# Kernel tuning notes

Measured on AMD Instinct MI355X. Metric: run time of the kernel, lower is better.

Reference implementation:

```python
import jax, jax.numpy as jnp
import numpy as np

N = 100000   # nodes
E = 3200000  # edges per graph
D = 16       # embedding_size, num_heads = 1
ATTN_SLOPE = 0.2   # DGL GATv2Conv negative_slope default
ACT_SLOPE = 0.01   # torch.nn.functional.leaky_relu default (activation arg)


def gatv2_layer(h, src, dst, W_src, b_src, W_dst, b_dst, attn):
    """DGL GATv2Conv with num_heads=1, activation=leaky_relu.
    h: [N, D]; src/dst: [E] int; W_*: [D, D]; b_*: [D]; attn: [D].
    """
    feat_src = h @ W_src + b_src          # [N, D]
    feat_dst = h @ W_dst + b_dst          # [N, D]
    el = feat_src[src]                    # [E, D] gather to edges
    e = jax.nn.leaky_relu(el + feat_dst[dst], ATTN_SLOPE)  # [E, D]
    score = e @ attn                      # [E] attention logits
    # segment softmax over incoming edges of each destination node
    smax = jax.ops.segment_max(score, dst, num_segments=N)
    smax = jnp.where(jnp.isfinite(smax), smax, 0.0)  # empty segments -> 0
    ex = jnp.exp(score - smax[dst])       # [E]
    denom = jax.ops.segment_sum(ex, dst, num_segments=N)  # [N]
    alpha = ex / denom[dst]               # [E]
    rst = jax.ops.segment_sum(alpha[:, None] * el, dst, num_segments=N)  # [N, D]
    return jax.nn.leaky_relu(rst, ACT_SLOPE)


def setup_inputs() -> dict:
    key = jax.random.key(0)
    ks = jax.random.split(key, 16)
    s = 1.0 / np.sqrt(D)
    return {
        "embedding": jax.random.normal(ks[0], (N, D), jnp.float32),
        "src1": jax.random.randint(ks[1], (E,), 0, N, jnp.int32),
        "dst1": jax.random.randint(ks[2], (E,), 0, N, jnp.int32),
        "src2": jax.random.randint(ks[3], (E,), 0, N, jnp.int32),
        "dst2": jax.random.randint(ks[4], (E,), 0, N, jnp.int32),
        "W_src1": jax.random.normal(ks[5], (D, D), jnp.float32) * s,
        "b_src1": jnp.zeros((D,), jnp.float32),
        "W_dst1": jax.random.normal(ks[6], (D, D), jnp.float32) * s,
        "b_dst1": jnp.zeros((D,), jnp.float32),
        "attn1": jax.random.normal(ks[7], (D,), jnp.float32) * s,
        "W_src2": jax.random.normal(ks[8], (D, D), jnp.float32) * s,
        "b_src2": jnp.zeros((D,), jnp.float32),
        "W_dst2": jax.random.normal(ks[9], (D, D), jnp.float32) * s,
        "b_dst2": jnp.zeros((D,), jnp.float32),
        "attn2": jax.random.normal(ks[10], (D,), jnp.float32) * s,
    }


def reference(embedding, src1, dst1, src2, dst2,
              W_src1, b_src1, W_dst1, b_dst1, attn1,
              W_src2, b_src2, W_dst2, b_dst2, attn2):
    user2item = gatv2_layer(embedding, src1, dst1, W_src1, b_src1, W_dst1, b_dst1, attn1)
    item_influence = gatv2_layer(user2item, src2, dst2, W_src2, b_src2, W_dst2, b_dst2, attn2)
    return item_influence  # [N, D]
```

## Files before the change

kernel.cpp:

```cpp
#include <hip/hip_runtime.h>
#include <hip/hip_fp16.h>

#define D 16
#define R 64
#define RBITS 6
#define RMASK 63
#define STRIDE 2560
#define CAP 2560
#define ACCT 512
#define KPT (CAP / ACCT)
#define EPB 16384
#define CHK 8192
#define K1T 1024
#define NB2 1664
#define ATTN_SLOPE 0.2f
#define ACT_SLOPE 0.01f

__device__ __forceinline__ float leaky_a(float v) {
    return v > 0.f ? v : ATTN_SLOPE * v;
}
__device__ __forceinline__ float2 h2f(unsigned u) {
    __half2 h = *(__half2*)&u;
    return __half22float2(h);
}


__device__ void binscatter_tile(int tile, const int* __restrict__ src,
                                const int* __restrict__ dst,
                                int* __restrict__ gcur, unsigned* __restrict__ binned,
                                int E, int NB, char* sb) {
    unsigned* sorted = (unsigned*)sb;
    unsigned short* sposb = (unsigned short*)(sb + 32768);
    int* soffs = (int*)(sb + 49152);
    int* wcur = (int*)(sb + 49152 + 4 * NB2);
    int* swsum = (int*)(sb + 49152 + 8 * NB2);
    int tid = threadIdx.x;
    int lane = tid & 63, w = tid >> 6;
    int base = tile * EPB;
    int count = E - base;
    if (count > EPB) count = EPB;

    for (int i = tid; i < NB; i += K1T) wcur[i] = 0;
    __syncthreads();

    if (count == EPB) {
        const int4* d4 = (const int4*)(dst + base);
#pragma unroll
        for (int m = 0; m < 4; m++) {
            int4 a = d4[m * K1T + tid];
            atomicAdd(&wcur[a.x >> RBITS], 1);
            atomicAdd(&wcur[a.y >> RBITS], 1);
            atomicAdd(&wcur[a.z >> RBITS], 1);
            atomicAdd(&wcur[a.w >> RBITS], 1);
        }
    } else {
        for (int k = 0; k < 16; k++) {
            int e = base + k * K1T + tid;
            if (e < E) atomicAdd(&wcur[dst[e] >> RBITS], 1);
        }
    }
    __syncthreads();

    for (int i = tid; i < NB; i += K1T) {
        int c = wcur[i];
        if (c > 0) {
            int res = atomicAdd(&gcur[i], c);
            wcur[i] = i * STRIDE + res;
        }
    }
    __syncthreads();

    int i0 = 2 * tid, i1 = 2 * tid + 1;
    for (int c = 0; c < 2; c++) {
        int cbase = base + c * CHK;
        int cc = count - c * CHK;
        if (cc <= 0) break;
        if (cc > CHK) cc = CHK;
        bool full = (cc == CHK);

        for (int i = tid; i < NB; i += K1T) soffs[i] = 0;
        __syncthreads();

        if (full) {
            const int4* d4 = (const int4*)(dst + cbase);
            int4 a = d4[tid], b4 = d4[K1T + tid];
            atomicAdd(&soffs[a.x >> RBITS], 1);
            atomicAdd(&soffs[a.y >> RBITS], 1);
            atomicAdd(&soffs[a.z >> RBITS], 1);
            atomicAdd(&soffs[a.w >> RBITS], 1);
            atomicAdd(&soffs[b4.x >> RBITS], 1);
            atomicAdd(&soffs[b4.y >> RBITS], 1);
            atomicAdd(&soffs[b4.z >> RBITS], 1);
            atomicAdd(&soffs[b4.w >> RBITS], 1);
        } else {
            for (int k = 0; k < 8; k++) {
                int e = cbase + k * K1T + tid;
                if (e < E) atomicAdd(&soffs[dst[e] >> RBITS], 1);
            }
        }
        __syncthreads();

        int a0 = (i0 < NB) ? soffs[i0] : 0;
        int a1 = (i1 < NB) ? soffs[i1] : 0;
        int pair = a0 + a1;
        int x = pair;
#pragma unroll
        for (int ofs = 1; ofs < 64; ofs <<= 1) {
            int y = __shfl_up(x, ofs, 64);
            if (lane >= ofs) x += y;
        }
        if (lane == 63) swsum[w] = x;
        __syncthreads();
        if (w == 0) {
            int v = (lane < 16) ? swsum[lane] : 0;
            int s = v;
#pragma unroll
            for (int ofs = 1; ofs < 16; ofs <<= 1) {
                int y = __shfl_up(s, ofs, 64);
                if (lane >= ofs) s += y;
            }
            if (lane < 16) swsum[lane] = s - v;
        }
        __syncthreads();
        int excl = x - pair + swsum[w];
        int e0 = excl, e1 = excl + a0;
        int d0v = 0, d1v = 0;
        if (i0 < NB) {
            soffs[i0] = e0;
            if (a0 > 0) { d0v = wcur[i0] - e0; wcur[i0] = d0v; }
        }
        if (i1 < NB) {
            soffs[i1] = e1;
            if (a1 > 0) { d1v = wcur[i1] - e1; wcur[i1] = d1v; }
        }
        __syncthreads();

        if (full) {
            const int4* d4 = (const int4*)(dst + cbase);
            const int4* s4 = (const int4*)(src + cbase);
            int4 a = d4[tid], b4 = d4[K1T + tid];
            int4 sa = s4[tid], sb4 = s4[K1T + tid];
            int dd[8] = {a.x, a.y, a.z, a.w, b4.x, b4.y, b4.z, b4.w};
            int ss[8] = {sa.x, sa.y, sa.z, sa.w, sb4.x, sb4.y, sb4.z, sb4.w};
#pragma unroll
            for (int m = 0; m < 8; m++) {
                int bb = dd[m] >> RBITS;
                int r = atomicAdd(&soffs[bb], 1);
                sorted[r] = ((unsigned)ss[m] << RBITS) | (unsigned)(dd[m] & RMASK);
                sposb[r] = (unsigned short)bb;
            }
        } else {
            for (int k = 0; k < 8; k++) {
                int e = cbase + k * K1T + tid;
                if (e < E) {
                    int dv = dst[e];
                    int bb = dv >> RBITS;
                    int r = atomicAdd(&soffs[bb], 1);
                    sorted[r] = ((unsigned)src[e] << RBITS) | (unsigned)(dv & RMASK);
                    sposb[r] = (unsigned short)bb;
                }
            }
        }
        __syncthreads();

#pragma unroll
        for (int m = 0; m < 8; m++) {
            int p = m * K1T + tid;
            if (p < cc) {
                int bb = sposb[p];
                int pos = p + wcur[bb];
                if (pos < (bb + 1) * STRIDE) binned[pos] = sorted[p];
            }
        }
        __syncthreads();

        if (c == 0) {
            if (i0 < NB && a0 > 0) wcur[i0] = d0v + e0 + a0;
            if (i1 < NB && a1 > 0) wcur[i1] = d1v + e1 + a1;
            __syncthreads();
        }
    }
}

__device__ void transform_tile(int tile, const float* __restrict__ h,
                               const float* __restrict__ Ws, const float* __restrict__ bs,
                               const float* __restrict__ Wd, const float* __restrict__ bd,
                               __half* __restrict__ fsh, float* __restrict__ fdst,
                               int N, char* sb) {
    float* sWs = (float*)sb;
    float* sWd = sWs + 256;
    float* sbs = sWd + 256;
    float* sbd = sbs + 16;
    int t = threadIdx.x;
    if (t < 256) { sWs[t] = Ws[t]; sWd[t] = Wd[t]; }
    if (t < 16) { sbs[t] = bs[t]; sbd[t] = bd[t]; }
    __syncthreads();
    int n = tile * K1T + t;
    if (n >= N) return;
    float hv[D];
    const float4* h4 = (const float4*)(h + (size_t)n * D);
#pragma unroll
    for (int k = 0; k < 4; k++) {
        float4 v = h4[k];
        hv[4 * k] = v.x; hv[4 * k + 1] = v.y; hv[4 * k + 2] = v.z; hv[4 * k + 3] = v.w;
    }
    float os[D], od[D];
#pragma unroll
    for (int d = 0; d < D; d++) {
        float ss = sbs[d];
        float sd = sbd[d];
#pragma unroll
        for (int k = 0; k < D; k++) {
            ss += hv[k] * sWs[k * D + d];
            sd += hv[k] * sWd[k * D + d];
        }
        os[d] = ss; od[d] = sd;
    }
    unsigned us[8];
#pragma unroll
    for (int k = 0; k < 8; k++) {
        __half2 hh = __floats2half2_rn(os[2 * k], os[2 * k + 1]);
        us[k] = *(unsigned*)&hh;
    }
    uint4* fo = (uint4*)(fsh + (size_t)n * D);
    fo[0] = make_uint4(us[0], us[1], us[2], us[3]);
    fo[1] = make_uint4(us[4], us[5], us[6], us[7]);
    float4* fd4 = (float4*)(fdst + (size_t)n * D);
#pragma unroll
    for (int k = 0; k < 4; k++)
        fd4[k] = make_float4(od[4 * k], od[4 * k + 1], od[4 * k + 2], od[4 * k + 3]);
}

__global__ void __launch_bounds__(K1T)
k1_kernel(const float* h, const float* Ws, const float* bs,
          const float* Wd, const float* bd,
          __half* fsh, float* fdst,
          const int* srcA, const int* dstA, int* gA, unsigned* binnedA, int EA,
          const int* srcB, const int* dstB, int* gB, unsigned* binnedB, int EB,
          int N, int NB, int B1, int B2, int TT) {
    __shared__ __align__(16) char sb[49152 + 8 * NB2 + 64];
    int bid = blockIdx.x;
    if (bid < B1) {
        binscatter_tile(bid, srcA, dstA, gA, binnedA, EA, NB, sb);
    } else if (bid < B1 + B2) {
        binscatter_tile(bid - B1, srcB, dstB, gB, binnedB, EB, NB, sb);
    } else {
        int t = bid - B1 - B2;
        if (t < TT) transform_tile(t, h, Ws, bs, Wd, bd, fsh, fdst, N, sb);
    }
}


template <bool DO_TAIL>
__global__ void __launch_bounds__(ACCT)
acc_kernel(const unsigned* __restrict__ binned, const int* __restrict__ gcur,
           const __half* __restrict__ fsh, const float* __restrict__ fdst,
           const float* __restrict__ attn, float* __restrict__ out,
           __half* __restrict__ fs2h, float* __restrict__ fd2,
           const float* __restrict__ Ws2, const float* __restrict__ bs2,
           const float* __restrict__ Wd2, const float* __restrict__ bd2,
           int N) {
    __shared__ float sfd[R * D];
    __shared__ int ebuf[CAP];
    __shared__ float exbuf[CAP];
    __shared__ int cstart[R + 1];
    __shared__ int cur[R];
    __shared__ float wtail[544];
    int b = blockIdx.x;
    int tid = threadIdx.x;
    int node0 = b * R;
    int nn = N - node0;
    if (nn > R) nn = R;
    for (int i = tid; i < nn * D; i += ACCT) sfd[i] = fdst[node0 * D + i];
    if (tid <= R) cstart[tid] = 0;
    if (DO_TAIL) {
        if (tid < 256) { wtail[tid] = Ws2[tid]; wtail[256 + tid] = Wd2[tid]; }
        if (tid < 16) { wtail[512 + tid] = bs2[tid]; wtail[528 + tid] = bd2[tid]; }
    }

    float av[D];
#pragma unroll
    for (int k = 0; k < D; k++) av[k] = attn[k];

    int cnt = gcur[b];
    if (cnt > CAP) cnt = CAP;
    int base = b * STRIDE;

    unsigned pls[KPT];
#pragma unroll
    for (int k = 0; k < KPT; k++) {
        int j = k * ACCT + tid;
        pls[k] = (j < cnt) ? binned[base + j] : 0xFFFFFFFFu;
    }
    __syncthreads();

    const uint4* fsh4 = (const uint4*)fsh;
    const uint2* fsq = (const uint2*)fsh;
    const float4* sfd4 = (const float4*)sfd;

#pragma unroll
    for (int k = 0; k < KPT; k++)
        if (pls[k] != 0xFFFFFFFFu) atomicAdd(&cstart[pls[k] & RMASK], 1);

    float exs[KPT];
#pragma unroll
    for (int k = 0; k + 1 < KPT; k += 2) {
        unsigned q0 = pls[k], q1 = pls[k + 1];
        uint4 ua0, ub0, ua1, ub1;
        if (q0 != 0xFFFFFFFFu) {
            int s = q0 >> RBITS;
            ua0 = fsh4[2 * s]; ub0 = fsh4[2 * s + 1];
        }
        if (q1 != 0xFFFFFFFFu) {
            int s = q1 >> RBITS;
            ua1 = fsh4[2 * s]; ub1 = fsh4[2 * s + 1];
        }
        if (q0 != 0xFFFFFFFFu) {
            int loc = q0 & RMASK;
            float4 f0 = sfd4[loc * 4 + 0], f1 = sfd4[loc * 4 + 1];
            float4 f2 = sfd4[loc * 4 + 2], f3 = sfd4[loc * 4 + 3];
            float2 c0 = h2f(ua0.x), c1 = h2f(ua0.y), c2 = h2f(ua0.z), c3 = h2f(ua0.w);
            float2 c4 = h2f(ub0.x), c5 = h2f(ub0.y), c6 = h2f(ub0.z), c7 = h2f(ub0.w);
            float p = leaky_a(c0.x + f0.x) * av[0]  + leaky_a(c0.y + f0.y) * av[1]
                    + leaky_a(c1.x + f0.z) * av[2]  + leaky_a(c1.y + f0.w) * av[3]
                    + leaky_a(c2.x + f1.x) * av[4]  + leaky_a(c2.y + f1.y) * av[5]
                    + leaky_a(c3.x + f1.z) * av[6]  + leaky_a(c3.y + f1.w) * av[7]
                    + leaky_a(c4.x + f2.x) * av[8]  + leaky_a(c4.y + f2.y) * av[9]
                    + leaky_a(c5.x + f2.z) * av[10] + leaky_a(c5.y + f2.w) * av[11]
                    + leaky_a(c6.x + f3.x) * av[12] + leaky_a(c6.y + f3.y) * av[13]
                    + leaky_a(c7.x + f3.z) * av[14] + leaky_a(c7.y + f3.w) * av[15];
            exs[k] = __expf(p);
        }
        if (q1 != 0xFFFFFFFFu) {
            int loc = q1 & RMASK;
            float4 f0 = sfd4[loc * 4 + 0], f1 = sfd4[loc * 4 + 1];
            float4 f2 = sfd4[loc * 4 + 2], f3 = sfd4[loc * 4 + 3];
            float2 c0 = h2f(ua1.x), c1 = h2f(ua1.y), c2 = h2f(ua1.z), c3 = h2f(ua1.w);
            float2 c4 = h2f(ub1.x), c5 = h2f(ub1.y), c6 = h2f(ub1.z), c7 = h2f(ub1.w);
            float p = leaky_a(c0.x + f0.x) * av[0]  + leaky_a(c0.y + f0.y) * av[1]
                    + leaky_a(c1.x + f0.z) * av[2]  + leaky_a(c1.y + f0.w) * av[3]
                    + leaky_a(c2.x + f1.x) * av[4]  + leaky_a(c2.y + f1.y) * av[5]
                    + leaky_a(c3.x + f1.z) * av[6]  + leaky_a(c3.y + f1.w) * av[7]
                    + leaky_a(c4.x + f2.x) * av[8]  + leaky_a(c4.y + f2.y) * av[9]
                    + leaky_a(c5.x + f2.z) * av[10] + leaky_a(c5.y + f2.w) * av[11]
                    + leaky_a(c6.x + f3.x) * av[12] + leaky_a(c6.y + f3.y) * av[13]
                    + leaky_a(c7.x + f3.z) * av[14] + leaky_a(c7.y + f3.w) * av[15];
            exs[k + 1] = __expf(p);
        }
    }
    if (KPT & 1) {
        unsigned q0 = pls[KPT - 1];
        if (q0 != 0xFFFFFFFFu) {
            int s = q0 >> RBITS;
            uint4 ua0 = fsh4[2 * s], ub0 = fsh4[2 * s + 1];
            int loc = q0 & RMASK;
            float4 f0 = sfd4[loc * 4 + 0], f1 = sfd4[loc * 4 + 1];
            float4 f2 = sfd4[loc * 4 + 2], f3 = sfd4[loc * 4 + 3];
            float2 c0 = h2f(ua0.x), c1 = h2f(ua0.y), c2 = h2f(ua0.z), c3 = h2f(ua0.w);
            float2 c4 = h2f(ub0.x), c5 = h2f(ub0.y), c6 = h2f(ub0.z), c7 = h2f(ub0.w);
            float p = leaky_a(c0.x + f0.x) * av[0]  + leaky_a(c0.y + f0.y) * av[1]
                    + leaky_a(c1.x + f0.z) * av[2]  + leaky_a(c1.y + f0.w) * av[3]
                    + leaky_a(c2.x + f1.x) * av[4]  + leaky_a(c2.y + f1.y) * av[5]
                    + leaky_a(c3.x + f1.z) * av[6]  + leaky_a(c3.y + f1.w) * av[7]
                    + leaky_a(c4.x + f2.x) * av[8]  + leaky_a(c4.y + f2.y) * av[9]
                    + leaky_a(c5.x + f2.z) * av[10] + leaky_a(c5.y + f2.w) * av[11]
                    + leaky_a(c6.x + f3.x) * av[12] + leaky_a(c6.y + f3.y) * av[13]
                    + leaky_a(c7.x + f3.z) * av[14] + leaky_a(c7.y + f3.w) * av[15];
            exs[KPT - 1] = __expf(p);
        }
    }
    __syncthreads();
    if (tid < R) {
        int v = cstart[tid];
        int x = v;
#pragma unroll
        for (int ofs = 1; ofs < 64; ofs <<= 1) {
            int y = __shfl_up(x, ofs, 64);
            if (tid >= ofs) x += y;
        }
        cstart[tid] = x - v;
        cur[tid] = x - v;
        if (tid == R - 1) cstart[R] = x;
    }
    __syncthreads();
#pragma unroll
    for (int k = 0; k < KPT; k++) {
        unsigned pl = pls[k];
        if (pl != 0xFFFFFFFFu) {
            int r = atomicAdd(&cur[pl & RMASK], 1);
            ebuf[r] = (int)pl;
            exbuf[r] = exs[k];
        }
    }
    __syncthreads();

    int lane = tid & 63;
    int w = tid >> 6;
    int q = lane & 3;
    int s2 = (lane >> 2) & 3;
    int n2 = lane >> 4;

    float4 acc[2];
    float den[2];
#pragma unroll
    for (int i = 0; i < 2; i++) {
        acc[i] = make_float4(0.f, 0.f, 0.f, 0.f);
        den[i] = 0.f;
    }
#pragma unroll
    for (int i = 0; i < 2; i++) {
        int loc = w * 8 + i * 4 + n2;
        int kb = cstart[loc], ke = cstart[loc + 1];
        int k = kb + s2;
        for (; k + 12 < ke; k += 16) {
            int pl0 = ebuf[k];
            int pl1 = ebuf[k + 4];
            int pl2 = ebuf[k + 8];
            int pl3 = ebuf[k + 12];
            float ex0 = exbuf[k];
            float ex1 = exbuf[k + 4];
            float ex2 = exbuf[k + 8];
            float ex3 = exbuf[k + 12];
            uint2 u0 = fsq[(((unsigned)pl0) >> RBITS) * 4 + q];
            uint2 u1 = fsq[(((unsigned)pl1) >> RBITS) * 4 + q];
            uint2 u2 = fsq[(((unsigned)pl2) >> RBITS) * 4 + q];
            uint2 u3 = fsq[(((unsigned)pl3) >> RBITS) * 4 + q];
            float2 a01 = h2f(u0.x), a23 = h2f(u0.y);
            float2 b01 = h2f(u1.x), b23 = h2f(u1.y);
            float2 c01 = h2f(u2.x), c23 = h2f(u2.y);
            float2 d01 = h2f(u3.x), d23 = h2f(u3.y);
            acc[i].x += ex0 * a01.x + ex1 * b01.x + ex2 * c01.x + ex3 * d01.x;
            acc[i].y += ex0 * a01.y + ex1 * b01.y + ex2 * c01.y + ex3 * d01.y;
            acc[i].z += ex0 * a23.x + ex1 * b23.x + ex2 * c23.x + ex3 * d23.x;
            acc[i].w += ex0 * a23.y + ex1 * b23.y + ex2 * c23.y + ex3 * d23.y;
            den[i] += (ex0 + ex1) + (ex2 + ex3);
        }
        for (; k < ke; k += 4) {
            int pl = ebuf[k];
            float ex = exbuf[k];
            uint2 u = fsq[(((unsigned)pl) >> RBITS) * 4 + q];
            float2 a01 = h2f(u.x), a23 = h2f(u.y);
            acc[i].x += ex * a01.x;
            acc[i].y += ex * a01.y;
            acc[i].z += ex * a23.x;
            acc[i].w += ex * a23.y;
            den[i] += ex;
        }
    }
#pragma unroll
    for (int i = 0; i < 2; i++) {
        float4 a = acc[i];
        float dn = den[i];
#pragma unroll
        for (int m = 4; m <= 8; m <<= 1) {
            a.x += __shfl_xor(a.x, m, 16);
            a.y += __shfl_xor(a.y, m, 16);
            a.z += __shfl_xor(a.z, m, 16);
            a.w += __shfl_xor(a.w, m, 16);
            dn += __shfl_xor(dn, m, 16);
        }
        int loc = w * 8 + i * 4 + n2;
        if (s2 == 0 && loc < nn) {
            float inv = dn > 0.f ? 1.f / dn : 0.f;
            float4 v;
            v.x = a.x * inv; v.x = v.x > 0.f ? v.x : ACT_SLOPE * v.x;
            v.y = a.y * inv; v.y = v.y > 0.f ? v.y : ACT_SLOPE * v.y;
            v.z = a.z * inv; v.z = v.z > 0.f ? v.z : ACT_SLOPE * v.z;
            v.w = a.w * inv; v.w = v.w > 0.f ? v.w : ACT_SLOPE * v.w;
            if (DO_TAIL) {
                *(float4*)&sfd[loc * D + q * 4] = v;
            } else {
                ((float4*)out)[(size_t)(node0 + loc) * 4 + q] = v;
            }
        }
    }
    if (DO_TAIL) {
        __syncthreads();
        int loc = tid >> 2, qq = tid & 3;
        if (tid < 256 && loc < nn) {
            float hvv[16];
#pragma unroll
            for (int k = 0; k < 16; k++) hvv[k] = sfd[loc * D + k];
            float s0 = wtail[512 + 4 * qq], s1 = wtail[513 + 4 * qq];
            float s2v = wtail[514 + 4 * qq], s3 = wtail[515 + 4 * qq];
            float d0 = wtail[528 + 4 * qq], d1 = wtail[529 + 4 * qq];
            float d2v = wtail[530 + 4 * qq], d3 = wtail[531 + 4 * qq];
#pragma unroll
            for (int k = 0; k < 16; k++) {
                float hk = hvv[k];
                const float* wr = &wtail[k * 16 + 4 * qq];
                const float* wr2 = &wtail[256 + k * 16 + 4 * qq];
                s0 += hk * wr[0]; s1 += hk * wr[1]; s2v += hk * wr[2]; s3 += hk * wr[3];
                d0 += hk * wr2[0]; d1 += hk * wr2[1]; d2v += hk * wr2[2]; d3 += hk * wr2[3];
            }
            __half2 p0 = __floats2half2_rn(s0, s1), p1 = __floats2half2_rn(s2v, s3);
            *(uint2*)(fs2h + (size_t)(node0 + loc) * D + 4 * qq) =
                make_uint2(*(unsigned*)&p0, *(unsigned*)&p1);
            *(float4*)(fd2 + (size_t)(node0 + loc) * D + 4 * qq) =
                make_float4(d0, d1, d2v, d3);
        }
    }
}


extern "C" void kernel_launch(void* const* d_in, const int* in_sizes, int n_in,
                              void* d_out, int out_size, void* d_ws, size_t ws_size,
                              hipStream_t stream) {
    const float* emb = (const float*)d_in[0];
    const int* src1 = (const int*)d_in[1];
    const int* dst1 = (const int*)d_in[2];
    const int* src2 = (const int*)d_in[3];
    const int* dst2 = (const int*)d_in[4];
    const float* Wsrc1 = (const float*)d_in[5];
    const float* bsrc1 = (const float*)d_in[6];
    const float* Wdst1 = (const float*)d_in[7];
    const float* bdst1 = (const float*)d_in[8];
    const float* attn1 = (const float*)d_in[9];
    const float* Wsrc2 = (const float*)d_in[10];
    const float* bsrc2 = (const float*)d_in[11];
    const float* Wdst2 = (const float*)d_in[12];
    const float* bdst2 = (const float*)d_in[13];
    const float* attn2 = (const float*)d_in[14];

    const int N = in_sizes[0] / D;
    const int E1 = in_sizes[1];
    const int E2 = in_sizes[3];
    const int NB = (N + R - 1) / R;
    const size_t ndf = (size_t)N * D;

    float* ws = (float*)d_ws;
    float* fd1 = ws;
    float* fd2 = fd1 + ndf;
    __half* fs1h = (__half*)(fd2 + ndf);
    __half* fs2h = fs1h + ndf;
    int* gA = (int*)(fs2h + ndf);
    int* gB = gA + NB2;
    unsigned* binned1 = (unsigned*)(gB + NB2);
    unsigned* binned2big = binned1 + (size_t)NB * STRIDE;
    size_t bigNeed = (size_t)((char*)(binned2big + (size_t)NB * STRIDE) - (char*)d_ws);
    bool big = ws_size >= bigNeed;
    (void)n_in; (void)out_size;

    const int B1 = (E1 + EPB - 1) / EPB;
    const int B2 = (E2 + EPB - 1) / EPB;
    const int TT = (N + K1T - 1) / K1T;

    (void)hipMemsetAsync(gA, 0, 2 * NB2 * sizeof(int), stream);

    if (big) {
        k1_kernel<<<B1 + B2 + TT, K1T, 0, stream>>>(
            emb, Wsrc1, bsrc1, Wdst1, bdst1, fs1h, fd1,
            src1, dst1, gA, binned1, E1,
            src2, dst2, gB, binned2big, E2,
            N, NB, B1, B2, TT);
        acc_kernel<true><<<NB, ACCT, 0, stream>>>(
            binned1, gA, fs1h, fd1, attn1, nullptr,
            fs2h, fd2, Wsrc2, bsrc2, Wdst2, bdst2, N);
        acc_kernel<false><<<NB, ACCT, 0, stream>>>(
            binned2big, gB, fs2h, fd2, attn2, (float*)d_out,
            nullptr, nullptr, nullptr, nullptr, nullptr, nullptr, N);
    } else {
        k1_kernel<<<B1 + TT, K1T, 0, stream>>>(
            emb, Wsrc1, bsrc1, Wdst1, bdst1, fs1h, fd1,
            src1, dst1, gA, binned1, E1,
            src2, dst2, gB, binned1, 0,
            N, NB, B1, 0, TT);
        acc_kernel<true><<<NB, ACCT, 0, stream>>>(
            binned1, gA, fs1h, fd1, attn1, nullptr,
            fs2h, fd2, Wsrc2, bsrc2, Wdst2, bdst2, N);
        k1_kernel<<<B2, K1T, 0, stream>>>(
            emb, Wsrc1, bsrc1, Wdst1, bdst1, fs1h, fd1,
            src2, dst2, gB, binned1, E2,
            src2, dst2, gB, binned1, 0,
            N, NB, B2, 0, 0);
        acc_kernel<false><<<NB, ACCT, 0, stream>>>(
            binned1, gB, fs2h, fd2, attn2, (float*)d_out,
            nullptr, nullptr, nullptr, nullptr, nullptr, nullptr, N);
    }
}
```

Baseline: 235.2 us.

## Halve binscatter block size and cache dst/src indices in registers

The binning kernel drops from 1024 to 512 threads per block, with a launch-bounds minimum of 4 blocks. Each thread now loads its 32 dst indices and 16 src indices per chunk once into registers and reuses them across the histogram and scatter passes, instead of re-reading them from global memory. The block-wide scan now gives each thread four bins, and each transform block handles 2048 nodes with a per-thread loop. Holding these arrays in registers raises register pressure, and with the launch-bounds limit this could cause spills.

```diff
diff --git a/kernel.cpp b/kernel.cpp
--- a/kernel.cpp
+++ b/kernel.cpp
@@ -11,7 +11,8 @@
 #define KPT (CAP / ACCT)
 #define EPB 16384
 #define CHK 8192
-#define K1T 1024
+#define K1T 512
+#define TNODES 2048
 #define NB2 1664
 #define ATTN_SLOPE 0.2f
 #define ACT_SLOPE 0.01f
@@ -39,22 +40,26 @@
     int base = tile * EPB;
     int count = E - base;
     if (count > EPB) count = EPB;
-
+    bool fullT = (count == EPB);
+
+    int dreg[32];
+    if (fullT) {
+        const int4* d4 = (const int4*)(dst + base);
+#pragma unroll
+        for (int m = 0; m < 8; m++) {
+            int4 a = d4[m * K1T + tid];
+            dreg[4 * m + 0] = a.x; dreg[4 * m + 1] = a.y;
+            dreg[4 * m + 2] = a.z; dreg[4 * m + 3] = a.w;
+        }
+    }
     for (int i = tid; i < NB; i += K1T) wcur[i] = 0;
     __syncthreads();
 
-    if (count == EPB) {
-        const int4* d4 = (const int4*)(dst + base);
-#pragma unroll
-        for (int m = 0; m < 4; m++) {
-            int4 a = d4[m * K1T + tid];
-            atomicAdd(&wcur[a.x >> RBITS], 1);
-            atomicAdd(&wcur[a.y >> RBITS], 1);
-            atomicAdd(&wcur[a.z >> RBITS], 1);
-            atomicAdd(&wcur[a.w >> RBITS], 1);
-        }
+    if (fullT) {
+#pragma unroll
+        for (int m = 0; m < 32; m++) atomicAdd(&wcur[dreg[m] >> RBITS], 1);
     } else {
-        for (int k = 0; k < 16; k++) {
+        for (int k = 0; k < 32; k++) {
             int e = base + k * K1T + tid;
             if (e < E) atomicAdd(&wcur[dst[e] >> RBITS], 1);
         }
@@ -70,30 +75,33 @@
     }
     __syncthreads();
 
-    int i0 = 2 * tid, i1 = 2 * tid + 1;
+    int i0 = 4 * tid;
     for (int c = 0; c < 2; c++) {
         int cbase = base + c * CHK;
         int cc = count - c * CHK;
         if (cc <= 0) break;
         if (cc > CHK) cc = CHK;
-        bool full = (cc == CHK);
-
+        bool fullC = fullT;
+
+        int sreg[16];
+        if (fullC) {
+            const int4* s4 = (const int4*)(src + cbase);
+#pragma unroll
+            for (int m2 = 0; m2 < 4; m2++) {
+                int4 a = s4[m2 * K1T + tid];
+                sreg[4 * m2 + 0] = a.x; sreg[4 * m2 + 1] = a.y;
+                sreg[4 * m2 + 2] = a.z; sreg[4 * m2 + 3] = a.w;
+            }
+        }
         for (int i = tid; i < NB; i += K1T) soffs[i] = 0;
         __syncthreads();
 
-        if (full) {
-            const int4* d4 = (const int4*)(dst + cbase);
-            int4 a = d4[tid], b4 = d4[K1T + tid];
-            atomicAdd(&soffs[a.x >> RBITS], 1);
-            atomicAdd(&soffs[a.y >> RBITS], 1);
-            atomicAdd(&soffs[a.z >> RBITS], 1);
-            atomicAdd(&soffs[a.w >> RBITS], 1);
-            atomicAdd(&soffs[b4.x >> RBITS], 1);
-            atomicAdd(&soffs[b4.y >> RBITS], 1);
-            atomicAdd(&soffs[b4.z >> RBITS], 1);
-            atomicAdd(&soffs[b4.w >> RBITS], 1);
+        if (fullC) {
+#pragma unroll
+            for (int mm = 0; mm < 16; mm++)
+                atomicAdd(&soffs[dreg[16 * c + mm] >> RBITS], 1);
         } else {
-            for (int k = 0; k < 8; k++) {
+            for (int k = 0; k < 16; k++) {
                 int e = cbase + k * K1T + tid;
                 if (e < E) atomicAdd(&soffs[dst[e] >> RBITS], 1);
             }
@@ -101,9 +109,11 @@
         __syncthreads();
 
         int a0 = (i0 < NB) ? soffs[i0] : 0;
-        int a1 = (i1 < NB) ? soffs[i1] : 0;
-        int pair = a0 + a1;
-        int x = pair;
+        int a1 = (i0 + 1 < NB) ? soffs[i0 + 1] : 0;
+        int a2 = (i0 + 2 < NB) ? soffs[i0 + 2] : 0;
+        int a3 = (i0 + 3 < NB) ? soffs[i0 + 3] : 0;
+        int quad = a0 + a1 + a2 + a3;
+        int x = quad;
 #pragma unroll
         for (int ofs = 1; ofs < 64; ofs <<= 1) {
             int y = __shfl_up(x, ofs, 64);
@@ -112,45 +122,48 @@
         if (lane == 63) swsum[w] = x;
         __syncthreads();
         if (w == 0) {
-            int v = (lane < 16) ? swsum[lane] : 0;
+            int v = (lane < 8) ? swsum[lane] : 0;
             int s = v;
 #pragma unroll
-            for (int ofs = 1; ofs < 16; ofs <<= 1) {
+            for (int ofs = 1; ofs < 8; ofs <<= 1) {
                 int y = __shfl_up(s, ofs, 64);
                 if (lane >= ofs) s += y;
             }
-            if (lane < 16) swsum[lane] = s - v;
-        }
-        __syncthreads();
-        int excl = x - pair + swsum[w];
-        int e0 = excl, e1 = excl + a0;
-        int d0v = 0, d1v = 0;
+            if (lane < 8) swsum[lane] = s - v;
+        }
+        __syncthreads();
+        int excl = x - quad + swsum[w];
+        int e0 = excl, e1 = e0 + a0, e2 = e1 + a1, e3 = e2 + a2;
+        int d0v = 0, d1v = 0, d2v = 0, d3v = 0;
         if (i0 < NB) {
             soffs[i0] = e0;
             if (a0 > 0) { d0v = wcur[i0] - e0; wcur[i0] = d0v; }
         }
-        if (i1 < NB) {
-            soffs[i1] = e1;
-            if (a1 > 0) { d1v = wcur[i1] - e1; wcur[i1] = d1v; }
-        }
-        __syncthreads();
-
-        if (full) {
-            const int4* d4 = (const int4*)(dst + cbase);
-            const int4* s4 = (const int4*)(src + cbase);
-            int4 a = d4[tid], b4 = d4[K1T + tid];
-            int4 sa = s4[tid], sb4 = s4[K1T + tid];
-            int dd[8] = {a.x, a.y, a.z, a.w, b4.x, b4.y, b4.z, b4.w};
-            int ss[8] = {sa.x, sa.y, sa.z, sa.w, sb4.x, sb4.y, sb4.z, sb4.w};
-#pragma unroll
-            for (int m = 0; m < 8; m++) {
-                int bb = dd[m] >> RBITS;
+        if (i0 + 1 < NB) {
+            soffs[i0 + 1] = e1;
+            if (a1 > 0) { d1v = wcur[i0 + 1] - e1; wcur[i0 + 1] = d1v; }
+        }
+        if (i0 + 2 < NB) {
+            soffs[i0 + 2] = e2;
+            if (a2 > 0) { d2v = wcur[i0 + 2] - e2; wcur[i0 + 2] = d2v; }
+        }
+        if (i0 + 3 < NB) {
+            soffs[i0 + 3] = e3;
+            if (a3 > 0) { d3v = wcur[i0 + 3] - e3; wcur[i0 + 3] = d3v; }
+        }
+        __syncthreads();
+
+        if (fullC) {
+#pragma unroll
+            for (int mm = 0; mm < 16; mm++) {
+                int dv = dreg[16 * c + mm];
+                int bb = dv >> RBITS;
                 int r = atomicAdd(&soffs[bb], 1);
-                sorted[r] = ((unsigned)ss[m] << RBITS) | (unsigned)(dd[m] & RMASK);
+                sorted[r] = ((unsigned)sreg[mm] << RBITS) | (unsigned)(dv & RMASK);
                 sposb[r] = (unsigned short)bb;
             }
         } else {
-            for (int k = 0; k < 8; k++) {
+            for (int k = 0; k < 16; k++) {
                 int e = cbase + k * K1T + tid;
                 if (e < E) {
                     int dv = dst[e];
@@ -164,8 +177,8 @@
         __syncthreads();
 
 #pragma unroll
-        for (int m = 0; m < 8; m++) {
-            int p = m * K1T + tid;
+        for (int mm = 0; mm < 16; mm++) {
+            int p = mm * K1T + tid;
             if (p < cc) {
                 int bb = sposb[p];
                 int pos = p + wcur[bb];
@@ -176,7 +189,9 @@
 
         if (c == 0) {
             if (i0 < NB && a0 > 0) wcur[i0] = d0v + e0 + a0;
-            if (i1 < NB && a1 > 0) wcur[i1] = d1v + e1 + a1;
+            if (i0 + 1 < NB && a1 > 0) wcur[i0 + 1] = d1v + e1 + a1;
+            if (i0 + 2 < NB && a2 > 0) wcur[i0 + 2] = d2v + e2 + a2;
+            if (i0 + 3 < NB && a3 > 0) wcur[i0 + 3] = d3v + e3 + a3;
             __syncthreads();
         }
     }
@@ -195,43 +210,46 @@
     if (t < 256) { sWs[t] = Ws[t]; sWd[t] = Wd[t]; }
     if (t < 16) { sbs[t] = bs[t]; sbd[t] = bd[t]; }
     __syncthreads();
-    int n = tile * K1T + t;
-    if (n >= N) return;
-    float hv[D];
-    const float4* h4 = (const float4*)(h + (size_t)n * D);
-#pragma unroll
-    for (int k = 0; k < 4; k++) {
-        float4 v = h4[k];
-        hv[4 * k] = v.x; hv[4 * k + 1] = v.y; hv[4 * k + 2] = v.z; hv[4 * k + 3] = v.w;
-    }
-    float os[D], od[D];
-#pragma unroll
-    for (int d = 0; d < D; d++) {
-        float ss = sbs[d];
-        float sd = sbd[d];
-#pragma unroll
-        for (int k = 0; k < D; k++) {
-            ss += hv[k] * sWs[k * D + d];
-            sd += hv[k] * sWd[k * D + d];
-        }
-        os[d] = ss; od[d] = sd;
-    }
-    unsigned us[8];
-#pragma unroll
-    for (int k = 0; k < 8; k++) {
-        __half2 hh = __floats2half2_rn(os[2 * k], os[2 * k + 1]);
-        us[k] = *(unsigned*)&hh;
-    }
-    uint4* fo = (uint4*)(fsh + (size_t)n * D);
-    fo[0] = make_uint4(us[0], us[1], us[2], us[3]);
-    fo[1] = make_uint4(us[4], us[5], us[6], us[7]);
-    float4* fd4 = (float4*)(fdst + (size_t)n * D);
-#pragma unroll
-    for (int k = 0; k < 4; k++)
-        fd4[k] = make_float4(od[4 * k], od[4 * k + 1], od[4 * k + 2], od[4 * k + 3]);
-}
-
-__global__ void __launch_bounds__(K1T)
+#pragma unroll
+    for (int kk = 0; kk < 4; kk++) {
+        int n = tile * TNODES + kk * K1T + t;
+        if (n >= N) break;
+        float hv[D];
+        const float4* h4 = (const float4*)(h + (size_t)n * D);
+#pragma unroll
+        for (int k = 0; k < 4; k++) {
+            float4 v = h4[k];
+            hv[4 * k] = v.x; hv[4 * k + 1] = v.y; hv[4 * k + 2] = v.z; hv[4 * k + 3] = v.w;
+        }
+        float os[D], od[D];
+#pragma unroll
+        for (int d = 0; d < D; d++) {
+            float ss = sbs[d];
+            float sd = sbd[d];
+#pragma unroll
+            for (int k = 0; k < D; k++) {
+                ss += hv[k] * sWs[k * D + d];
+                sd += hv[k] * sWd[k * D + d];
+            }
+            os[d] = ss; od[d] = sd;
+        }
+        unsigned us[8];
+#pragma unroll
+        for (int k = 0; k < 8; k++) {
+            __half2 hh = __floats2half2_rn(os[2 * k], os[2 * k + 1]);
+            us[k] = *(unsigned*)&hh;
+        }
+        uint4* fo = (uint4*)(fsh + (size_t)n * D);
+        fo[0] = make_uint4(us[0], us[1], us[2], us[3]);
+        fo[1] = make_uint4(us[4], us[5], us[6], us[7]);
+        float4* fd4 = (float4*)(fdst + (size_t)n * D);
+#pragma unroll
+        for (int k = 0; k < 4; k++)
+            fd4[k] = make_float4(od[4 * k], od[4 * k + 1], od[4 * k + 2], od[4 * k + 3]);
+    }
+}
+
+__global__ void __launch_bounds__(K1T, 4)
 k1_kernel(const float* h, const float* Ws, const float* bs,
           const float* Wd, const float* bd,
           __half* fsh, float* fdst,
@@ -543,7 +561,7 @@
 
     const int B1 = (E1 + EPB - 1) / EPB;
     const int B2 = (E2 + EPB - 1) / EPB;
-    const int TT = (N + K1T - 1) / K1T;
+    const int TT = (N + TNODES - 1) / TNODES;
 
     (void)hipMemsetAsync(gA, 0, 2 * NB2 * sizeof(int), stream);
 
```

Result: slower. 292.0 us (+24.1%).

## Fuse all stages into one cooperative persistent kernel with grid syncs

Applied to the files above, without the earlier changes.

Replaces the memset plus three kernel launches with a single cooperative mega-kernel. It zeroes the counters, runs the binscatter and transform tiles, then both accumulation passes, separated by grid-wide syncs, and processes two 64-node buckets per 1024-thread block through a split shared-memory layout. This removes launch gaps and tail effects between stages. The trade-off is a persistent grid capped at 512 blocks, which may limit parallelism and occupancy. The larger shared footprint and grid barriers add cost, and a non-cooperative multi-launch fallback is kept.

```diff
diff --git a/kernel.cpp b/kernel.cpp
--- a/kernel.cpp
+++ b/kernel.cpp
@@ -1,5 +1,8 @@
 #include <hip/hip_runtime.h>
 #include <hip/hip_fp16.h>
+#include <hip/hip_cooperative_groups.h>
+
+namespace cg = cooperative_groups;
 
 #define D 16
 #define R 64
@@ -13,6 +16,7 @@
 #define CHK 8192
 #define K1T 1024
 #define NB2 1664
+#define SLICE 25600
 #define ATTN_SLOPE 0.2f
 #define ACT_SLOPE 0.01f
 
@@ -196,84 +200,72 @@
     if (t < 16) { sbs[t] = bs[t]; sbd[t] = bd[t]; }
     __syncthreads();
     int n = tile * K1T + t;
-    if (n >= N) return;
-    float hv[D];
-    const float4* h4 = (const float4*)(h + (size_t)n * D);
-#pragma unroll
-    for (int k = 0; k < 4; k++) {
-        float4 v = h4[k];
-        hv[4 * k] = v.x; hv[4 * k + 1] = v.y; hv[4 * k + 2] = v.z; hv[4 * k + 3] = v.w;
-    }
-    float os[D], od[D];
-#pragma unroll
-    for (int d = 0; d < D; d++) {
-        float ss = sbs[d];
-        float sd = sbd[d];
-#pragma unroll
-        for (int k = 0; k < D; k++) {
-            ss += hv[k] * sWs[k * D + d];
-            sd += hv[k] * sWd[k * D + d];
-        }
-        os[d] = ss; od[d] = sd;
-    }
-    unsigned us[8];
-#pragma unroll
-    for (int k = 0; k < 8; k++) {
-        __half2 hh = __floats2half2_rn(os[2 * k], os[2 * k + 1]);
-        us[k] = *(unsigned*)&hh;
-    }
-    uint4* fo = (uint4*)(fsh + (size_t)n * D);
-    fo[0] = make_uint4(us[0], us[1], us[2], us[3]);
-    fo[1] = make_uint4(us[4], us[5], us[6], us[7]);
-    float4* fd4 = (float4*)(fdst + (size_t)n * D);
-#pragma unroll
-    for (int k = 0; k < 4; k++)
-        fd4[k] = make_float4(od[4 * k], od[4 * k + 1], od[4 * k + 2], od[4 * k + 3]);
-}
-
-__global__ void __launch_bounds__(K1T)
-k1_kernel(const float* h, const float* Ws, const float* bs,
-          const float* Wd, const float* bd,
-          __half* fsh, float* fdst,
-          const int* srcA, const int* dstA, int* gA, unsigned* binnedA, int EA,
-          const int* srcB, const int* dstB, int* gB, unsigned* binnedB, int EB,
-          int N, int NB, int B1, int B2, int TT) {
-    __shared__ __align__(16) char sb[49152 + 8 * NB2 + 64];
-    int bid = blockIdx.x;
-    if (bid < B1) {
-        binscatter_tile(bid, srcA, dstA, gA, binnedA, EA, NB, sb);
-    } else if (bid < B1 + B2) {
-        binscatter_tile(bid - B1, srcB, dstB, gB, binnedB, EB, NB, sb);
-    } else {
-        int t = bid - B1 - B2;
-        if (t < TT) transform_tile(t, h, Ws, bs, Wd, bd, fsh, fdst, N, sb);
-    }
+    if (n < N) {
+        float hv[D];
+        const float4* h4 = (const float4*)(h + (size_t)n * D);
+#pragma unroll
+        for (int k = 0; k < 4; k++) {
+            float4 v = h4[k];
+            hv[4 * k] = v.x; hv[4 * k + 1] = v.y; hv[4 * k + 2] = v.z; hv[4 * k + 3] = v.w;
+        }
+        float os[D], od[D];
+#pragma unroll
+        for (int d = 0; d < D; d++) {
+            float ss = sbs[d];
+            float sd = sbd[d];
+#pragma unroll
+            for (int k = 0; k < D; k++) {
+                ss += hv[k] * sWs[k * D + d];
+                sd += hv[k] * sWd[k * D + d];
+            }
+            os[d] = ss; od[d] = sd;
+        }
+        unsigned us[8];
+#pragma unroll
+        for (int k = 0; k < 8; k++) {
+            __half2 hh = __floats2half2_rn(os[2 * k], os[2 * k + 1]);
+            us[k] = *(unsigned*)&hh;
+        }
+        uint4* fo = (uint4*)(fsh + (size_t)n * D);
+        fo[0] = make_uint4(us[0], us[1], us[2], us[3]);
+        fo[1] = make_uint4(us[4], us[5], us[6], us[7]);
+        float4* fd4 = (float4*)(fdst + (size_t)n * D);
+#pragma unroll
+        for (int k = 0; k < 4; k++)
+            fd4[k] = make_float4(od[4 * k], od[4 * k + 1], od[4 * k + 2], od[4 * k + 3]);
+    }
+    __syncthreads();
 }
 
 
 template <bool DO_TAIL>
-__global__ void __launch_bounds__(ACCT)
-acc_kernel(const unsigned* __restrict__ binned, const int* __restrict__ gcur,
-           const __half* __restrict__ fsh, const float* __restrict__ fdst,
-           const float* __restrict__ attn, float* __restrict__ out,
-           __half* __restrict__ fs2h, float* __restrict__ fd2,
-           const float* __restrict__ Ws2, const float* __restrict__ bs2,
-           const float* __restrict__ Wd2, const float* __restrict__ bd2,
-           int N) {
-    __shared__ float sfd[R * D];
-    __shared__ int ebuf[CAP];
-    __shared__ float exbuf[CAP];
-    __shared__ int cstart[R + 1];
-    __shared__ int cur[R];
-    __shared__ float wtail[544];
-    int b = blockIdx.x;
-    int tid = threadIdx.x;
+__device__ void acc_pair(int pb, const unsigned* __restrict__ binned,
+                         const int* __restrict__ gcur,
+                         const __half* __restrict__ fsh, const float* __restrict__ fdst,
+                         const float* __restrict__ attn, float* __restrict__ out,
+                         __half* __restrict__ fs2h, float* __restrict__ fd2,
+                         const float* __restrict__ Ws2, const float* __restrict__ bs2,
+                         const float* __restrict__ Wd2, const float* __restrict__ bd2,
+                         int N, char* sb) {
+    int tidf = threadIdx.x;
+    int sub = tidf >> 9;
+    int tid = tidf & 511;
+    int b = pb * 2 + sub;
+    char* my = sb + sub * SLICE;
+    float* sfd = (float*)my;
+    int* ebuf = (int*)(my + 4096);
+    float* exbuf = (float*)(my + 14336);
+    int* cstart = (int*)(my + 24576);
+    int* cur = (int*)(my + 24836);
+    float* wtail = (float*)(sb + 2 * SLICE);
+
     int node0 = b * R;
     int nn = N - node0;
     if (nn > R) nn = R;
+    if (nn < 0) nn = 0;
     for (int i = tid; i < nn * D; i += ACCT) sfd[i] = fdst[node0 * D + i];
     if (tid <= R) cstart[tid] = 0;
-    if (DO_TAIL) {
+    if (DO_TAIL && sub == 0) {
         if (tid < 256) { wtail[tid] = Ws2[tid]; wtail[256 + tid] = Wd2[tid]; }
         if (tid < 16) { wtail[512 + tid] = bs2[tid]; wtail[528 + tid] = bd2[tid]; }
     }
@@ -500,6 +492,89 @@
                 make_float4(d0, d1, d2v, d3);
         }
     }
+    __syncthreads();
+}
+
+
+struct MegaP {
+    const float* h;
+    const float *Ws1, *bs1, *Wd1, *bd1, *attn1;
+    const float *Ws2, *bs2, *Wd2, *bd2, *attn2;
+    __half* fs1h; float* fd1; __half* fs2h; float* fd2;
+    const int *src1, *dst1; int* gA; unsigned* binned1;
+    const int *src2, *dst2; int* gB; unsigned* binned2;
+    float* out;
+    int N, NB, E1, E2, B1, B2a, B2b, TT, nPairs;
+};
+
+__global__ void __launch_bounds__(1024, 8)
+mega_kernel(MegaP p) {
+    __shared__ __align__(16) char sb[49152 + 8 * NB2 + 64];
+    cg::grid_group grid = cg::this_grid();
+    int tid = threadIdx.x, bid = blockIdx.x, nblk = gridDim.x;
+
+    for (int i = bid * 1024 + tid; i < 2 * NB2; i += nblk * 1024) p.gA[i] = 0;
+    grid.sync();
+
+    int T1 = p.B1 + p.B2a + p.TT;
+    for (int t = bid; t < T1; t += nblk) {
+        if (t < p.B1)
+            binscatter_tile(t, p.src1, p.dst1, p.gA, p.binned1, p.E1, p.NB, sb);
+        else if (t < p.B1 + p.B2a)
+            binscatter_tile(t - p.B1, p.src2, p.dst2, p.gB, p.binned2, p.E2, p.NB, sb);
+        else
+            transform_tile(t - p.B1 - p.B2a, p.h, p.Ws1, p.bs1, p.Wd1, p.bd1,
+                           p.fs1h, p.fd1, p.N, sb);
+    }
+    grid.sync();
+
+    for (int pb = bid; pb < p.nPairs; pb += nblk)
+        acc_pair<true>(pb, p.binned1, p.gA, p.fs1h, p.fd1, p.attn1, nullptr,
+                       p.fs2h, p.fd2, p.Ws2, p.bs2, p.Wd2, p.bd2, p.N, sb);
+    grid.sync();
+
+    for (int t = bid; t < p.B2b; t += nblk)
+        binscatter_tile(t, p.src2, p.dst2, p.gB, p.binned2, p.E2, p.NB, sb);
+    grid.sync();
+
+    for (int pb = bid; pb < p.nPairs; pb += nblk)
+        acc_pair<false>(pb, p.binned2, p.gB, p.fs2h, p.fd2, p.attn2, p.out,
+                        nullptr, nullptr, nullptr, nullptr, nullptr, nullptr, p.N, sb);
+}
+
+
+__global__ void __launch_bounds__(K1T)
+k1_kernel(const float* h, const float* Ws, const float* bs,
+          const float* Wd, const float* bd,
+          __half* fsh, float* fdst,
+          const int* srcA, const int* dstA, int* gA, unsigned* binnedA, int EA,
+          const int* srcB, const int* dstB, int* gB, unsigned* binnedB, int EB,
+          int N, int NB, int B1, int B2, int TT) {
+    __shared__ __align__(16) char sb[49152 + 8 * NB2 + 64];
+    int bid = blockIdx.x;
+    if (bid < B1) {
+        binscatter_tile(bid, srcA, dstA, gA, binnedA, EA, NB, sb);
+    } else if (bid < B1 + B2) {
+        binscatter_tile(bid - B1, srcB, dstB, gB, binnedB, EB, NB, sb);
+    } else {
+        int t = bid - B1 - B2;
+        if (t < TT) transform_tile(t, h, Ws, bs, Wd, bd, fsh, fdst, N, sb);
+    }
+}
+
+template <bool DO_TAIL>
+__global__ void __launch_bounds__(1024)
+acc_kernel(const unsigned* __restrict__ binned, const int* __restrict__ gcur,
+           const __half* __restrict__ fsh, const float* __restrict__ fdst,
+           const float* __restrict__ attn, float* __restrict__ out,
+           __half* __restrict__ fs2h, float* __restrict__ fd2,
+           const float* __restrict__ Ws2, const float* __restrict__ bs2,
+           const float* __restrict__ Wd2, const float* __restrict__ bd2,
+           int N, int nPairs) {
+    __shared__ __align__(16) char sb[2 * SLICE + 2176];
+    if (blockIdx.x < (unsigned)nPairs)
+        acc_pair<DO_TAIL>(blockIdx.x, binned, gcur, fsh, fdst, attn, out,
+                          fs2h, fd2, Ws2, bs2, Wd2, bd2, N, sb);
 }
 
 
@@ -544,37 +619,64 @@
     const int B1 = (E1 + EPB - 1) / EPB;
     const int B2 = (E2 + EPB - 1) / EPB;
     const int TT = (N + K1T - 1) / K1T;
-
-    (void)hipMemsetAsync(gA, 0, 2 * NB2 * sizeof(int), stream);
-
-    if (big) {
-        k1_kernel<<<B1 + B2 + TT, K1T, 0, stream>>>(
-            emb, Wsrc1, bsrc1, Wdst1, bdst1, fs1h, fd1,
-            src1, dst1, gA, binned1, E1,
-            src2, dst2, gB, binned2big, E2,
-            N, NB, B1, B2, TT);
-        acc_kernel<true><<<NB, ACCT, 0, stream>>>(
-            binned1, gA, fs1h, fd1, attn1, nullptr,
-            fs2h, fd2, Wsrc2, bsrc2, Wdst2, bdst2, N);
-        acc_kernel<false><<<NB, ACCT, 0, stream>>>(
-            binned2big, gB, fs2h, fd2, attn2, (float*)d_out,
-            nullptr, nullptr, nullptr, nullptr, nullptr, nullptr, N);
-    } else {
-        k1_kernel<<<B1 + TT, K1T, 0, stream>>>(
-            emb, Wsrc1, bsrc1, Wdst1, bdst1, fs1h, fd1,
-            src1, dst1, gA, binned1, E1,
-            src2, dst2, gB, binned1, 0,
-            N, NB, B1, 0, TT);
-        acc_kernel<true><<<NB, ACCT, 0, stream>>>(
-            binned1, gA, fs1h, fd1, attn1, nullptr,
-            fs2h, fd2, Wsrc2, bsrc2, Wdst2, bdst2, N);
-        k1_kernel<<<B2, K1T, 0, stream>>>(
-            emb, Wsrc1, bsrc1, Wdst1, bdst1, fs1h, fd1,
-            src2, dst2, gB, binned1, E2,
-            src2, dst2, gB, binned1, 0,
-            N, NB, B2, 0, 0);
-        acc_kernel<false><<<NB, ACCT, 0, stream>>>(
-            binned1, gB, fs2h, fd2, attn2, (float*)d_out,
-            nullptr, nullptr, nullptr, nullptr, nullptr, nullptr, N);
-    }
-}
+    const int nPairs = (NB + 1) / 2;
+
+    MegaP prm;
+    prm.h = emb;
+    prm.Ws1 = Wsrc1; prm.bs1 = bsrc1; prm.Wd1 = Wdst1; prm.bd1 = bdst1; prm.attn1 = attn1;
+    prm.Ws2 = Wsrc2; prm.bs2 = bsrc2; prm.Wd2 = Wdst2; prm.bd2 = bdst2; prm.attn2 = attn2;
+    prm.fs1h = fs1h; prm.fd1 = fd1; prm.fs2h = fs2h; prm.fd2 = fd2;
+    prm.src1 = src1; prm.dst1 = dst1; prm.gA = gA; prm.binned1 = binned1;
+    prm.src2 = src2; prm.dst2 = dst2; prm.gB = gB;
+    prm.binned2 = big ? binned2big : binned1;
+    prm.out = (float*)d_out;
+    prm.N = N; prm.NB = NB; prm.E1 = E1; prm.E2 = E2;
+    prm.B1 = B1; prm.B2a = big ? B2 : 0; prm.B2b = big ? 0 : B2;
+    prm.TT = TT; prm.nPairs = nPairs;
+
+    int maxBlk = 0;
+    (void)hipOccupancyMaxActiveBlocksPerMultiprocessor(&maxBlk, (const void*)mega_kernel, 1024, 0);
+    int gridc = maxBlk * 256;
+    if (gridc > 512) gridc = 512;
+
+    hipError_t err = hipErrorUnknown;
+    if (gridc >= 1) {
+        void* args[] = {(void*)&prm};
+        err = hipLaunchCooperativeKernel((const void*)mega_kernel, dim3(gridc),
+                                         dim3(1024), args, 0, stream);
+    }
+    if (err != hipSuccess) {
+        (void)hipGetLastError();
+        (void)hipMemsetAsync(gA, 0, 2 * NB2 * sizeof(int), stream);
+        if (big) {
+            k1_kernel<<<B1 + B2 + TT, K1T, 0, stream>>>(
+                emb, Wsrc1, bsrc1, Wdst1, bdst1, fs1h, fd1,
+                src1, dst1, gA, binned1, E1,
+                src2, dst2, gB, binned2big, E2,
+                N, NB, B1, B2, TT);
+            acc_kernel<true><<<nPairs, 1024, 0, stream>>>(
+                binned1, gA, fs1h, fd1, attn1, nullptr,
+                fs2h, fd2, Wsrc2, bsrc2, Wdst2, bdst2, N, nPairs);
+            acc_kernel<false><<<nPairs, 1024, 0, stream>>>(
+                binned2big, gB, fs2h, fd2, attn2, (float*)d_out,
+                nullptr, nullptr, nullptr, nullptr, nullptr, nullptr, N, nPairs);
+        } else {
+            k1_kernel<<<B1 + TT, K1T, 0, stream>>>(
+                emb, Wsrc1, bsrc1, Wdst1, bdst1, fs1h, fd1,
+                src1, dst1, gA, binned1, E1,
+                src2, dst2, gB, binned1, 0,
+                N, NB, B1, 0, TT);
+            acc_kernel<true><<<nPairs, 1024, 0, stream>>>(
+                binned1, gA, fs1h, fd1, attn1, nullptr,
+                fs2h, fd2, Wsrc2, bsrc2, Wdst2, bdst2, N, nPairs);
+            k1_kernel<<<B2, K1T, 0, stream>>>(
+                emb, Wsrc1, bsrc1, Wdst1, bdst1, fs1h, fd1,
+                src2, dst2, gB, binned1, E2,
+                src2, dst2, gB, binned1, 0,
+                N, NB, B2, 0, 0);
+            acc_kernel<false><<<nPairs, 1024, 0, stream>>>(
+                binned1, gB, fs2h, fd2, attn2, (float*)d_out,
+                nullptr, nullptr, nullptr, nullptr, nullptr, nullptr, N, nPairs);
+        }
+    }
+}
```

Result: slower. 323.3 us (+37.4%).
